# Performance work log

Hardware: AMD Instinct MI355X
Metric: run time of the kernel (lower is better)

Reference implementation:

```python
import jax, jax.numpy as jnp
import numpy as np

EPS = 1e-5
DN = ('NCHW', 'OIHW', 'NCHW')


def conv3x3(x, w, b):
    y = jax.lax.conv_general_dilated(x, w, window_strides=(1, 1), padding='SAME',
                                     dimension_numbers=DN)
    return y + b[None, :, None, None]


def bn_relu(x, g, be, m, v):
    # inference-mode BatchNorm2d followed by ReLU, folded into one FMA
    inv = g / jnp.sqrt(v + EPS)
    return jax.nn.relu(x * inv[None, :, None, None] + (be - m * inv)[None, :, None, None])


def haar_idwt2(cA, cH, cV, cD):
    # pywt.idwt2(coeffs, 'db1'): cH = detail along rows (axis -2), cV = detail along cols (axis -1)
    # Exact Haar synthesis -> 2x2 pixel blocks (pixel-shuffle style, no CPU round-trip)
    p00 = (cA + cH + cV + cD) * 0.5  # (2i,   2j)
    p01 = (cA + cH - cV - cD) * 0.5  # (2i,   2j+1)
    p10 = (cA - cH + cV - cD) * 0.5  # (2i+1, 2j)
    p11 = (cA - cH - cV + cD) * 0.5  # (2i+1, 2j+1)
    B, C, H, W = cA.shape
    even = jnp.stack([p00, p01], axis=-1).reshape(B, C, H, 2 * W)
    odd = jnp.stack([p10, p11], axis=-1).reshape(B, C, H, 2 * W)
    return jnp.stack([even, odd], axis=-2).reshape(B, C, 2 * H, 2 * W)


def setup_inputs() -> dict:
    key = jax.random.key(0)
    ks = jax.random.split(key, 24)
    B, IN_C, OUT_C, H, W = 16, 128, 64, 64, 64
    d = {}
    d['x'] = jax.random.normal(ks[0], (B, IN_C, H, W), jnp.float32)
    d['s'] = jax.random.normal(ks[1], (B, OUT_C, 2 * H, 2 * W), jnp.float32)
    # input_convdwt: Conv(in_c -> 4*in_c) + BN
    d['w1'] = jax.random.normal(ks[2], (4 * IN_C, IN_C, 3, 3), jnp.float32) * 0.05
    d['b1'] = jax.random.normal(ks[3], (4 * IN_C,), jnp.float32) * 0.05
    d['g1'] = jax.random.uniform(ks[4], (4 * IN_C,), jnp.float32, 0.5, 1.5)
    d['be1'] = jax.random.normal(ks[5], (4 * IN_C,), jnp.float32) * 0.05
    d['m1'] = jax.random.normal(ks[6], (4 * IN_C,), jnp.float32) * 0.05
    d['v1'] = jax.random.uniform(ks[7], (4 * IN_C,), jnp.float32, 0.5, 1.5)
    # s_con: Conv(in_c -> out_c) + BN
    d['ws'] = jax.random.normal(ks[8], (OUT_C, IN_C, 3, 3), jnp.float32) * 0.05
    d['bs'] = jax.random.normal(ks[9], (OUT_C,), jnp.float32) * 0.05
    d['gs'] = jax.random.uniform(ks[10], (OUT_C,), jnp.float32, 0.5, 1.5)
    d['bes'] = jax.random.normal(ks[11], (OUT_C,), jnp.float32) * 0.05
    d['ms'] = jax.random.normal(ks[12], (OUT_C,), jnp.float32) * 0.05
    d['vs'] = jax.random.uniform(ks[13], (OUT_C,), jnp.float32, 0.5, 1.5)
    # conv: Conv(in_c -> out_c) + BN (applied to concat(s, s_out))
    d['w2'] = jax.random.normal(ks[14], (OUT_C, IN_C, 3, 3), jnp.float32) * 0.05
    d['b2'] = jax.random.normal(ks[15], (OUT_C,), jnp.float32) * 0.05
    d['g2'] = jax.random.uniform(ks[16], (OUT_C,), jnp.float32, 0.5, 1.5)
    d['be2'] = jax.random.normal(ks[17], (OUT_C,), jnp.float32) * 0.05
    d['m2'] = jax.random.normal(ks[18], (OUT_C,), jnp.float32) * 0.05
    d['v2'] = jax.random.uniform(ks[19], (OUT_C,), jnp.float32, 0.5, 1.5)
    return d


def reference(x, s, w1, b1, g1, be1, m1, v1,
              ws, bs, gs, bes, ms, vs,
              w2, b2, g2, be2, m2, v2):
    # input_convdwt: conv -> BN -> ReLU, channels in_c -> 4*in_c
    h = bn_relu(conv3x3(x, w1, b1), g1, be1, m1, v1)
    c = h.shape[1]
    q = c // 4
    cA, cH, cV, cD = h[:, :q], h[:, q:2 * q], h[:, 2 * q:3 * q], h[:, 3 * q:]
    idwt_out = haar_idwt2(cA, cH, cV, cD)  # (B, in_c, 2H, 2W)
    # skip-connection branch (s is not None)
    s_out = bn_relu(conv3x3(idwt_out, ws, bs), gs, bes, ms, vs)  # (B, out_c, 2H, 2W)
    concat = jnp.concatenate([s, s_out], axis=1)                  # (B, in_c, 2H, 2W)
    decoder_output = bn_relu(conv3x3(concat, w2, b2), g2, be2, m2, v2)
    return decoder_output
```

## Files before the change

### kernel.cpp

```cpp
#include <hip/hip_runtime.h>
#include <hip/hip_bf16.h>

typedef __attribute__((ext_vector_type(8))) short short8;
typedef __attribute__((ext_vector_type(4))) float f32x4;
typedef unsigned short u16;

#define EPSV 1e-5f

__device__ __forceinline__ u16 f2bf(float f) {
    __hip_bfloat16 h = __float2bfloat16(f);
    return *reinterpret_cast<u16*>(&h);
}

#define GLOAD_LDS16(g, l)                                                      \
    __builtin_amdgcn_global_load_lds(                                          \
        (const __attribute__((address_space(1))) void*)(g),                    \
        (__attribute__((address_space(3))) void*)(l), 16, 0, 0)

__global__ void cvt_fused_kernel(const float* __restrict__ x, u16* __restrict__ xb,
                                 const float* __restrict__ s, u16* __restrict__ sb) {
    int b = blockIdx.x;
    const float* src; u16* dst; int C, H, W, u;
    if (b < 4096) { src = x; dst = xb; C = 128; H = 64;  W = 64;  u = b * 256 + threadIdx.x; if (u >= 1048576) return; }
    else          { src = s; dst = sb; C = 64;  H = 128; W = 128; u = (b - 4096) * 256 + threadIdx.x; if (u >= 2097152) return; }
    int kb = u & 3;
    int p  = u >> 2;
    int xx = p % W;  p /= W;
    int yy = p % H;  p /= H;
    int n  = p & 15;
    int cc = p >> 4;
    short8 v;
#pragma unroll
    for (int j = 0; j < 8; ++j)
        v[j] = (short)f2bf(src[(((size_t)n * C + cc * 32 + kb * 8 + j) * H + yy) * W + xx]);
    *(short8*)(dst + ((((size_t)cc * 16 + n) * H + yy) * W + xx) * 32 + kb * 8) = v;
}

__global__ void repack_fused_kernel(const float* __restrict__ w1, const float* __restrict__ ws,
                                    const float* __restrict__ w2, u16* __restrict__ wf1,
                                    u16* __restrict__ wfS, u16* __restrict__ wf2) {
    int b = blockIdx.x;
    if (b < 288) {
        int u = b * 256 + threadIdx.x;
        if (u >= 4 * 8 * 9 * 4 * 64) return;
        int l = u & 63;
        int r = u >> 6;
        int ciC = r & 3;  r >>= 2;
        int t   = r % 9;  r /= 9;
        int bt  = r & 7;
        int cc  = r >> 3;
        int co  = (bt >> 1) * 128 + cc * 32 + (bt & 1) * 16 + (l & 15);
        int ci0 = ciC * 32 + (l >> 4) * 8;
        short8 v;
#pragma unroll
        for (int e = 0; e < 8; ++e)
            v[e] = (short)f2bf(w1[((size_t)co * 128 + ci0 + e) * 9 + t]);
        *(short8*)(wf1 + (size_t)u * 8) = v;
    } else {
        int g = b - 288;
        const float* w = (g < 36) ? ws : w2;
        u16* wf        = (g < 36) ? wfS : wf2;
        int u = (g % 36) * 256 + threadIdx.x;
        if (u >= 4 * 9 * 4 * 64) return;
        int l = u & 63;
        int r = u >> 6;
        int ciC = r & 3;  r >>= 2;
        int t   = r % 9;
        int bt  = r / 9;
        int co  = bt * 16 + (l & 15);
        int ci0 = ciC * 32 + (l >> 4) * 8;
        short8 v;
#pragma unroll
        for (int e = 0; e < 8; ++e)
            v[e] = (short)f2bf(w[((size_t)co * 128 + ci0 + e) * 9 + t]);
        *(short8*)(wf + (size_t)u * 8) = v;
    }
}

__global__ __launch_bounds__(256, 2)
void conv1_mfma_kernel(const u16* __restrict__ inb, const u16* __restrict__ wf,
                       const float* __restrict__ bb, const float* __restrict__ gg,
                       const float* __restrict__ bee, const float* __restrict__ mm,
                       const float* __restrict__ vv, u16* __restrict__ ob) {
    const int tile = blockIdx.x;
    const int cc   = blockIdx.y;
    const int n    = blockIdx.z;
    const int x0   = (tile & 3) * 16;
    const int y0   = (tile >> 2) * 8;
    const int tid  = threadIdx.x;
    const int lane = tid & 63;
    const int wid  = tid >> 6;
    const int wm   = wid >> 1;
    const int wc   = wid & 1;
    const int kb   = lane >> 4;
    const int xl   = lane & 15;

    __shared__ float4 lds4[720];
    __shared__ float4 wlds[2][1536];
    const short8* ldsr  = (const short8*)lds4;
    const short8* wldsr = (const short8*)wlds;

    f32x4 acc[4][4];
#pragma unroll
    for (int j = 0; j < 4; ++j)
#pragma unroll
        for (int q = 0; q < 4; ++q) acc[j][q] = (f32x4){0.f, 0.f, 0.f, 0.f};

    float4 sreg[3];
    auto load_stage = [&](int ciC) {
#pragma unroll
        for (int p = 0; p < 3; ++p) {
            int e = p * 256 + tid;
            float4 v = make_float4(0.f, 0.f, 0.f, 0.f);
            if (e < 720) {
                int pix = e >> 2, ke = e & 3;
                int yy = pix / 18;
                int xx = pix - yy * 18;
                int gy = y0 - 1 + yy, gx = x0 - 1 + xx;
                if ((unsigned)gy < 64u && (unsigned)gx < 64u)
                    v = *(const float4*)(inb + ((((size_t)ciC * 16 + n) * 64 + gy) * 64 + gx) * 32 + ke * 8);
            }
            sreg[p] = v;
        }
    };
    auto write_stage = [&]() {
#pragma unroll
        for (int p = 0; p < 3; ++p) {
            int e = p * 256 + tid;
            if (e < 720) lds4[e ^ ((e >> 2) & 7)] = sreg[p];
        }
    };
    auto stage_w = [&](int ciC, int dx, int buf) {
#pragma unroll
        for (int i = 0; i < 6; ++i) {
            int seg = wid * 6 + i;
            int bt  = seg / 3;
            int dy  = seg - bt * 3;
            int t   = dy * 3 + dx;
            const u16* gp = wf + (size_t)((cc * 8 + bt) * 9 + t) * 2048 + ciC * 512 + lane * 8;
            GLOAD_LDS16(gp, &wlds[buf][seg * 64]);
        }
    };

    load_stage(0);
    stage_w(0, 0, 0);
    for (int ciC = 0; ciC < 4; ++ciC) {
        write_stage();
        asm volatile("s_waitcnt lgkmcnt(0)" ::: "memory");
        __builtin_amdgcn_s_barrier();
        __builtin_amdgcn_sched_barrier(0);
        if (ciC < 3) load_stage(ciC + 1);
#pragma unroll
        for (int dx = 0; dx < 3; ++dx) {
            const int cur = (ciC + dx) & 1;
            if (dx == 0) {
                if (ciC < 3) asm volatile("s_waitcnt vmcnt(3)" ::: "memory");
                else         asm volatile("s_waitcnt vmcnt(0)" ::: "memory");
            } else {
                asm volatile("s_waitcnt vmcnt(0)" ::: "memory");
            }
            __builtin_amdgcn_sched_barrier(0);
            __builtin_amdgcn_s_barrier();
            __builtin_amdgcn_sched_barrier(0);
            if (dx < 2)        stage_w(ciC, dx + 1, cur ^ 1);
            else if (ciC < 3)  stage_w(ciC + 1, 0, cur ^ 1);

            short8 a[6];
#pragma unroll
            for (int r = 0; r < 6; ++r) {
                int pix = (wm * 4 + r) * 18 + xl + dx;
                int e = pix * 4 + kb;
                a[r] = ldsr[e ^ ((e >> 2) & 7)];
            }
            __builtin_amdgcn_s_setprio(1);
#pragma unroll
            for (int dy = 0; dy < 3; ++dy) {
                short8 b[4];
#pragma unroll
                for (int q = 0; q < 4; ++q) {
                    int bt = q * 2 + wc;
                    b[q] = wldsr[cur * 1536 + (bt * 3 + dy) * 64 + lane];
                }
#pragma unroll
                for (int j = 0; j < 4; ++j)
#pragma unroll
                    for (int q = 0; q < 4; ++q)
                        acc[j][q] = __builtin_amdgcn_mfma_f32_16x16x32_bf16(a[j + dy], b[q], acc[j][q], 0, 0, 0);
            }
            __builtin_amdgcn_s_setprio(0);
        }
        __builtin_amdgcn_s_barrier();
    }

    float invq[4], shq[4];
#pragma unroll
    for (int q = 0; q < 4; ++q) {
        int co  = q * 128 + cc * 32 + wc * 16 + xl;
        float inv = gg[co] / sqrtf(vv[co] + EPSV);
        invq[q] = inv;
        shq[q]  = bb[co] * inv + bee[co] - mm[co] * inv;
    }
    const int c32 = wc * 16 + xl;
#pragma unroll
    for (int j = 0; j < 4; ++j) {
        int y = y0 + wm * 4 + j;
#pragma unroll
        for (int i = 0; i < 4; ++i) {
            float A_ = fmaxf(acc[j][0][i] * invq[0] + shq[0], 0.f);
            float H_ = fmaxf(acc[j][1][i] * invq[1] + shq[1], 0.f);
            float V_ = fmaxf(acc[j][2][i] * invq[2] + shq[2], 0.f);
            float D_ = fmaxf(acc[j][3][i] * invq[3] + shq[3], 0.f);
            float p00 = (A_ + H_ + V_ + D_) * 0.5f;
            float p01 = (A_ + H_ - V_ - D_) * 0.5f;
            float p10 = (A_ - H_ + V_ - D_) * 0.5f;
            float p11 = (A_ - H_ - V_ + D_) * 0.5f;
            int oy = 2 * y, ox = 2 * (x0 + kb * 4 + i);
            size_t base = ((((size_t)cc * 16 + n) * 128 + oy) * 128 + ox) * 32 + c32;
            ob[base]            = f2bf(p00);
            ob[base + 32]       = f2bf(p01);
            ob[base + 128 * 32] = f2bf(p10);
            ob[base + 128 * 32 + 32] = f2bf(p11);
        }
    }
}

template <bool FP32OUT>
__global__ __launch_bounds__(256, 2)
void convg_mfma_kernel(const u16* __restrict__ inb, const u16* __restrict__ wf,
                       const float* __restrict__ bb, const float* __restrict__ gg,
                       const float* __restrict__ bee, const float* __restrict__ mm,
                       const float* __restrict__ vv, u16* __restrict__ ob,
                       float* __restrict__ of) {
    const int tile = blockIdx.x;
    const int n    = blockIdx.y;
    const int x0   = (tile & 7) * 16;
    const int y0   = (tile >> 3) * 8;
    const int tid  = threadIdx.x;
    const int lane = tid & 63;
    const int wid  = tid >> 6;
    const int wm   = wid >> 1;
    const int wc   = wid & 1;
    const int kb   = lane >> 4;
    const int xl   = lane & 15;

    __shared__ float4 lds4[720];
    const short8* ldsr = (const short8*)lds4;

    f32x4 acc[4][2];
#pragma unroll
    for (int j = 0; j < 4; ++j)
#pragma unroll
        for (int cb = 0; cb < 2; ++cb) acc[j][cb] = (f32x4){0.f, 0.f, 0.f, 0.f};

    float4 sreg[3];
    auto load_stage = [&](int ciC) {
#pragma unroll
        for (int p = 0; p < 3; ++p) {
            int e = p * 256 + tid;
            float4 v = make_float4(0.f, 0.f, 0.f, 0.f);
            if (e < 720) {
                int pix = e >> 2, ke = e & 3;
                int yy = pix / 18;
                int xx = pix - yy * 18;
                int gy = y0 - 1 + yy, gx = x0 - 1 + xx;
                if ((unsigned)gy < 128u && (unsigned)gx < 128u)
                    v = *(const float4*)(inb + ((((size_t)ciC * 16 + n) * 128 + gy) * 128 + gx) * 32 + ke * 8);
            }
            sreg[p] = v;
        }
    };
    auto write_stage = [&]() {
#pragma unroll
        for (int p = 0; p < 3; ++p) {
            int e = p * 256 + tid;
            if (e < 720) lds4[e ^ ((e >> 2) & 7)] = sreg[p];
        }
    };

    load_stage(0);
    for (int ciC = 0; ciC < 4; ++ciC) {
        write_stage();
        __syncthreads();
        if (ciC < 3) load_stage(ciC + 1);
#pragma unroll
        for (int dx = 0; dx < 3; ++dx) {
            short8 a[6];
#pragma unroll
            for (int r = 0; r < 6; ++r) {
                int pix = (wm * 4 + r) * 18 + xl + dx;
                int e = pix * 4 + kb;
                a[r] = ldsr[e ^ ((e >> 2) & 7)];
            }
#pragma unroll
            for (int dy = 0; dy < 3; ++dy) {
                const int t = dy * 3 + dx;
                short8 b[2];
#pragma unroll
                for (int cb = 0; cb < 2; ++cb) {
                    int bt = wc * 2 + cb;
                    b[cb] = *(const short8*)(wf + ((size_t)((bt * 9 + t) * 4 + ciC) * 64 + lane) * 8);
                }
#pragma unroll
                for (int j = 0; j < 4; ++j)
#pragma unroll
                    for (int cb = 0; cb < 2; ++cb)
                        acc[j][cb] = __builtin_amdgcn_mfma_f32_16x16x32_bf16(a[j + dy], b[cb], acc[j][cb], 0, 0, 0);
            }
        }
        __syncthreads();
    }

#pragma unroll
    for (int cb = 0; cb < 2; ++cb) {
        int co = (wc * 2 + cb) * 16 + xl;
        float inv = gg[co] / sqrtf(vv[co] + EPSV);
        float sh  = bb[co] * inv + bee[co] - mm[co] * inv;
#pragma unroll
        for (int j = 0; j < 4; ++j) {
            int y = y0 + wm * 4 + j;
            if (FP32OUT) {
                float4 v4;
                v4.x = fmaxf(acc[j][cb][0] * inv + sh, 0.f);
                v4.y = fmaxf(acc[j][cb][1] * inv + sh, 0.f);
                v4.z = fmaxf(acc[j][cb][2] * inv + sh, 0.f);
                v4.w = fmaxf(acc[j][cb][3] * inv + sh, 0.f);
                *(float4*)&of[(((size_t)n * 64 + co) * 128 + y) * 128 + x0 + kb * 4] = v4;
            } else {
#pragma unroll
                for (int i = 0; i < 4; ++i) {
                    float val = fmaxf(acc[j][cb][i] * inv + sh, 0.f);
                    int xg = x0 + kb * 4 + i;
                    ob[((((size_t)(co >> 5) * 16 + n) * 128 + y) * 128 + xg) * 32 + (co & 31)] = f2bf(val);
                }
            }
        }
    }
}

extern "C" void kernel_launch(void* const* d_in, const int* in_sizes, int n_in,
                              void* d_out, int out_size, void* d_ws, size_t ws_size,
                              hipStream_t stream) {
    const float* x   = (const float*)d_in[0];
    const float* s   = (const float*)d_in[1];
    const float* w1  = (const float*)d_in[2];
    const float* b1  = (const float*)d_in[3];
    const float* g1  = (const float*)d_in[4];
    const float* be1 = (const float*)d_in[5];
    const float* m1  = (const float*)d_in[6];
    const float* v1  = (const float*)d_in[7];
    const float* wsw = (const float*)d_in[8];
    const float* bs  = (const float*)d_in[9];
    const float* gs  = (const float*)d_in[10];
    const float* bes = (const float*)d_in[11];
    const float* ms  = (const float*)d_in[12];
    const float* vs  = (const float*)d_in[13];
    const float* w2  = (const float*)d_in[14];
    const float* b2  = (const float*)d_in[15];
    const float* g2  = (const float*)d_in[16];
    const float* be2 = (const float*)d_in[17];
    const float* m2  = (const float*)d_in[18];
    const float* v2  = (const float*)d_in[19];
    float* out = (float*)d_out;

    char* wsp = (char*)d_ws;
    u16* xb   = (u16*)(wsp);
    u16* idwt = (u16*)(wsp + 16777216);
    u16* cat  = (u16*)(wsp + 16777216 + 67108864);
    u16* wf1  = (u16*)(wsp + 16777216 + 67108864 + 67108864);
    u16* wfS  = (u16*)(wsp + 16777216 + 67108864 + 67108864 + 1179648);
    u16* wf2  = (u16*)(wsp + 16777216 + 67108864 + 67108864 + 1179648 + 147456);

    cvt_fused_kernel<<<dim3(12288), dim3(256), 0, stream>>>(x, xb, s, cat);
    repack_fused_kernel<<<dim3(360), dim3(256), 0, stream>>>(w1, wsw, w2, wf1, wfS, wf2);

    conv1_mfma_kernel<<<dim3(32, 4, 16), dim3(256), 0, stream>>>(
        xb, wf1, b1, g1, be1, m1, v1, idwt);

    convg_mfma_kernel<false><<<dim3(128, 16), dim3(256), 0, stream>>>(
        idwt, wfS, bs, gs, bes, ms, vs,
        cat + (size_t)2 * 16 * 128 * 128 * 32, nullptr);

    convg_mfma_kernel<true><<<dim3(128, 16), dim3(256), 0, stream>>>(
        cat, wf2, b2, g2, be2, m2, v2, nullptr, out);
}
```

Before: 209.0 us.

## Switch convg kernel to 32x32x16 MFMA with repacked weight fragments

Rewrites the second and third 3x3 conv kernels to use 32x32x16 bf16 MFMA instead of 16x16x32, with each wave covering 32 pixels (two rows of 16) by all 64 output channels. The weight prepack is changed to match the 32-wide fragment layout, and the epilogue mapping is updated. The goal is fewer MFMA issues and fewer LDS A-fragment reads per FLOP. The cost is a different register footprint and bank-access pattern. Separately, it removes the s_setprio hints around the MFMA loop in conv1.

```diff
diff --git a/kernel.cpp b/kernel.cpp
--- a/kernel.cpp
+++ b/kernel.cpp
@@ -3,6 +3,7 @@
 
 typedef __attribute__((ext_vector_type(8))) short short8;
 typedef __attribute__((ext_vector_type(4))) float f32x4;
+typedef __attribute__((ext_vector_type(16))) float f32x16;
 typedef unsigned short u16;
 
 #define EPSV 1e-5f
@@ -61,14 +62,15 @@
         const float* w = (g < 36) ? ws : w2;
         u16* wf        = (g < 36) ? wfS : wf2;
         int u = (g % 36) * 256 + threadIdx.x;
-        if (u >= 4 * 9 * 4 * 64) return;
+        if (u >= 2 * 9 * 4 * 2 * 64) return;
         int l = u & 63;
         int r = u >> 6;
+        int kin = r & 1;  r >>= 1;
         int ciC = r & 3;  r >>= 2;
         int t   = r % 9;
-        int bt  = r / 9;
-        int co  = bt * 16 + (l & 15);
-        int ci0 = ciC * 32 + (l >> 4) * 8;
+        int bt2 = r / 9;
+        int co  = bt2 * 32 + (l & 31);
+        int ci0 = ciC * 32 + kin * 16 + (l >> 5) * 8;
         short8 v;
 #pragma unroll
         for (int e = 0; e < 8; ++e)
@@ -172,7 +174,6 @@
                 int e = pix * 4 + kb;
                 a[r] = ldsr[e ^ ((e >> 2) & 7)];
             }
-            __builtin_amdgcn_s_setprio(1);
 #pragma unroll
             for (int dy = 0; dy < 3; ++dy) {
                 short8 b[4];
@@ -187,7 +188,6 @@
                     for (int q = 0; q < 4; ++q)
                         acc[j][q] = __builtin_amdgcn_mfma_f32_16x16x32_bf16(a[j + dy], b[q], acc[j][q], 0, 0, 0);
             }
-            __builtin_amdgcn_s_setprio(0);
         }
         __builtin_amdgcn_s_barrier();
     }
@@ -238,19 +238,19 @@
     const int tid  = threadIdx.x;
     const int lane = tid & 63;
     const int wid  = tid >> 6;
-    const int wm   = wid >> 1;
-    const int wc   = wid & 1;
-    const int kb   = lane >> 4;
-    const int xl   = lane & 15;
+    const int row  = lane & 31;
+    const int kh   = lane >> 5;
+    const int px   = row & 15;
+    const int py   = row >> 4;
 
     __shared__ float4 lds4[720];
     const short8* ldsr = (const short8*)lds4;
 
-    f32x4 acc[4][2];
-#pragma unroll
-    for (int j = 0; j < 4; ++j)
-#pragma unroll
-        for (int cb = 0; cb < 2; ++cb) acc[j][cb] = (f32x4){0.f, 0.f, 0.f, 0.f};
+    f32x16 acc[2];
+#pragma unroll
+    for (int b2 = 0; b2 < 2; ++b2)
+#pragma unroll
+        for (int e = 0; e < 16; ++e) acc[b2][e] = 0.f;
 
     float4 sreg[3];
     auto load_stage = [&](int ciC) {
@@ -284,53 +284,52 @@
         if (ciC < 3) load_stage(ciC + 1);
 #pragma unroll
         for (int dx = 0; dx < 3; ++dx) {
-            short8 a[6];
-#pragma unroll
-            for (int r = 0; r < 6; ++r) {
-                int pix = (wm * 4 + r) * 18 + xl + dx;
-                int e = pix * 4 + kb;
-                a[r] = ldsr[e ^ ((e >> 2) & 7)];
-            }
+            short8 a[3][2];
+#pragma unroll
+            for (int dy = 0; dy < 3; ++dy)
+#pragma unroll
+                for (int kin = 0; kin < 2; ++kin) {
+                    int pix = (wid * 2 + py + dy) * 18 + px + dx;
+                    int e = pix * 4 + kin * 2 + kh;
+                    a[dy][kin] = ldsr[e ^ ((e >> 2) & 7)];
+                }
 #pragma unroll
             for (int dy = 0; dy < 3; ++dy) {
                 const int t = dy * 3 + dx;
-                short8 b[2];
-#pragma unroll
-                for (int cb = 0; cb < 2; ++cb) {
-                    int bt = wc * 2 + cb;
-                    b[cb] = *(const short8*)(wf + ((size_t)((bt * 9 + t) * 4 + ciC) * 64 + lane) * 8);
-                }
-#pragma unroll
-                for (int j = 0; j < 4; ++j)
-#pragma unroll
-                    for (int cb = 0; cb < 2; ++cb)
-                        acc[j][cb] = __builtin_amdgcn_mfma_f32_16x16x32_bf16(a[j + dy], b[cb], acc[j][cb], 0, 0, 0);
+#pragma unroll
+                for (int kin = 0; kin < 2; ++kin)
+#pragma unroll
+                    for (int b2 = 0; b2 < 2; ++b2) {
+                        short8 b = *(const short8*)(wf + ((size_t)((((b2 * 9 + t) * 4 + ciC) * 2) + kin) * 64 + lane) * 8);
+                        acc[b2] = __builtin_amdgcn_mfma_f32_32x32x16_bf16(a[dy][kin], b, acc[b2], 0, 0, 0);
+                    }
             }
         }
         __syncthreads();
     }
 
 #pragma unroll
-    for (int cb = 0; cb < 2; ++cb) {
-        int co = (wc * 2 + cb) * 16 + xl;
+    for (int b2 = 0; b2 < 2; ++b2) {
+        int co = b2 * 32 + (lane & 31);
         float inv = gg[co] / sqrtf(vv[co] + EPSV);
         float sh  = bb[co] * inv + bee[co] - mm[co] * inv;
 #pragma unroll
-        for (int j = 0; j < 4; ++j) {
-            int y = y0 + wm * 4 + j;
+        for (int g = 0; g < 4; ++g) {
+            int rbase = g * 8 + kh * 4;
+            int xg = x0 + (rbase & 15);
+            int yg = y0 + wid * 2 + (rbase >> 4);
             if (FP32OUT) {
                 float4 v4;
-                v4.x = fmaxf(acc[j][cb][0] * inv + sh, 0.f);
-                v4.y = fmaxf(acc[j][cb][1] * inv + sh, 0.f);
-                v4.z = fmaxf(acc[j][cb][2] * inv + sh, 0.f);
-                v4.w = fmaxf(acc[j][cb][3] * inv + sh, 0.f);
-                *(float4*)&of[(((size_t)n * 64 + co) * 128 + y) * 128 + x0 + kb * 4] = v4;
+                v4.x = fmaxf(acc[b2][g * 4 + 0] * inv + sh, 0.f);
+                v4.y = fmaxf(acc[b2][g * 4 + 1] * inv + sh, 0.f);
+                v4.z = fmaxf(acc[b2][g * 4 + 2] * inv + sh, 0.f);
+                v4.w = fmaxf(acc[b2][g * 4 + 3] * inv + sh, 0.f);
+                *(float4*)&of[(((size_t)n * 64 + co) * 128 + yg) * 128 + xg] = v4;
             } else {
 #pragma unroll
                 for (int i = 0; i < 4; ++i) {
-                    float val = fmaxf(acc[j][cb][i] * inv + sh, 0.f);
-                    int xg = x0 + kb * 4 + i;
-                    ob[((((size_t)(co >> 5) * 16 + n) * 128 + y) * 128 + xg) * 32 + (co & 31)] = f2bf(val);
+                    float val = fmaxf(acc[b2][g * 4 + i] * inv + sh, 0.f);
+                    ob[((((size_t)b2 * 16 + n) * 128 + yg) * 128 + xg + i) * 32 + (co & 31)] = f2bf(val);
                 }
             }
         }
```

Measured after the change: 227.2 us. +8.7%, slower.
